# Kernel optimization log

Hardware: AMD Instinct MI355X
Metric: run time of the kernel (lower is better)

Reference implementation:

```python
import jax, jax.numpy as jnp
import numpy as np

B, C, H, W = 32, 512, 32, 32
K = 1024  # num_embeddings


def setup_inputs() -> dict:
    key = jax.random.key(0)
    k1, k2 = jax.random.split(key)
    z = jax.random.normal(k1, (B, C, H, W), dtype=jnp.float32)
    embedding = jax.random.normal(k2, (K, C), dtype=jnp.float32)
    return {"z": z, "embedding": embedding}


def reference(z, embedding):
    # NCHW -> NHWC, flatten to [N, C]
    zt = jnp.transpose(z, (0, 2, 3, 1))            # [B, H, W, C]
    z_flat = zt.reshape(-1, zt.shape[-1])          # [N, C]
    # squared-euclidean distances: ||z||^2 - 2 z.e^T + ||e||^2
    dist = (jnp.sum(z_flat ** 2, axis=1, keepdims=True)
            - 2.0 * z_flat @ embedding.T
            + jnp.sum(embedding ** 2, axis=1))     # [N, K]
    indices = jnp.argmin(dist, axis=1)             # [N]
    quantized = embedding[indices].reshape(zt.shape)  # [B, H, W, C]
    quantized = jnp.transpose(quantized, (0, 3, 1, 2))  # [B, C, H, W]
    return quantized, indices.reshape(z.shape[0], -1)
```

## Files before the change

### kernel.cpp

```cpp
#include <hip/hip_runtime.h>
#include <hip/hip_bf16.h>

#define CDIM 512
#define KDIM 1024
#define HW   1024
#define NPOS 32768
#define BM   128
#define BN   128
#define BK   64
#define NKS  (CDIM / BK)
#define NNB  (KDIM / BN)
#define TILE_USHORT (8 * 128 * 8)

typedef float  f32x16 __attribute__((ext_vector_type(16)));
typedef float  f4     __attribute__((ext_vector_type(4)));
typedef short  bf16x8 __attribute__((ext_vector_type(8)));
typedef unsigned int u32x4 __attribute__((ext_vector_type(4)));

static __device__ __forceinline__ unsigned short f2bf(float f) {
    __hip_bfloat16 h = __float2bfloat16(f);
    union { __hip_bfloat16 h; unsigned short u; } cv; cv.h = h; return cv.u;
}
static __device__ __forceinline__ float bf2f(unsigned short u) {
    union { unsigned short u; __hip_bfloat16 h; } cv; cv.u = u; return __bfloat162float(cv.h);
}

__global__ __launch_bounds__(64) void prep_e(const float* __restrict__ e,
                                             unsigned short* __restrict__ Bt_hi,
                                             unsigned short* __restrict__ Bt_lo,
                                             float* __restrict__ enorm) {
    const int k  = blockIdx.x;
    const int t  = threadIdx.x;
    const int nb = k >> 7, row = k & 127;
    const int ks = t >> 3, slot = t & 7;

    const f4* src = (const f4*)(e + (size_t)k * CDIM + ks * 64 + slot * 8);
    const f4 a = src[0], b = src[1];
    float v[8] = {a.x, a.y, a.z, a.w, b.x, b.y, b.z, b.w};

    unsigned int hw_[4], lw_[4];
    float ss = 0.0f;
    #pragma unroll
    for (int d = 0; d < 4; ++d) {
        const float v0 = v[2 * d], v1 = v[2 * d + 1];
        const unsigned short h0 = f2bf(v0), h1 = f2bf(v1);
        hw_[d] = (unsigned int)h0 | ((unsigned int)h1 << 16);
        lw_[d] = (unsigned int)f2bf(v0 - bf2f(h0)) |
                 ((unsigned int)f2bf(v1 - bf2f(h1)) << 16);
        ss += v0 * v0 + v1 * v1;
    }
    const size_t off = ((((size_t)nb * 8 + ks) * 8 + slot) * 128 + row) * 8;
    *(u32x4*)(Bt_hi + off) = u32x4{hw_[0], hw_[1], hw_[2], hw_[3]};
    *(u32x4*)(Bt_lo + off) = u32x4{lw_[0], lw_[1], lw_[2], lw_[3]};

    #pragma unroll
    for (int o = 32; o > 0; o >>= 1) ss += __shfl_down(ss, o, 64);
    if (t == 0) enorm[k] = ss;
}

__global__ __launch_bounds__(256) void vq_gemm(const float* __restrict__ z,
                                               const unsigned short* __restrict__ Bt_hi,
                                               const unsigned short* __restrict__ Bt_lo,
                                               const float* __restrict__ enorm,
                                               float2* __restrict__ part) {
    __shared__ unsigned short Ah[8][128][8], Al[8][128][8];
    __shared__ unsigned short Bh[8][128][8], Bl[8][128][8];
    __shared__ float lval[2][128];
    __shared__ int   lidx[2][128];

    const int bid = blockIdx.x;
    const int x = bid & 7, jj = bid >> 3;
    const int m  = x * 32 + (jj >> 3);
    const int nb = jj & 7;

    const int n0  = m * BM;
    const int b   = n0 >> 10;
    const int hw0 = n0 & 1023;

    const int t   = threadIdx.x;
    const int wid = t >> 6, l = t & 63;
    const int wr  = wid >> 1, wc = wid & 1;

    f32x16 acc[2][2];
    #pragma unroll
    for (int i = 0; i < 2; ++i)
        #pragma unroll
        for (int j = 0; j < 2; ++j) acc[i][j] = (f32x16)0.0f;

    const float* zbase = z + (size_t)b * CDIM * HW + hw0;
    const int sp = t & 127;
    const int sh = t >> 7;

    for (int ks = 0; ks < NKS; ++ks) {
        float v[32];
        const float* zc = zbase + (size_t)(ks * 64 + sh * 32) * HW + sp;
        #pragma unroll
        for (int i = 0; i < 32; ++i) v[i] = zc[(size_t)i * HW];
        u32x4 bhv[4], blv[4];
        const u32x4* bsh = (const u32x4*)(Bt_hi + ((size_t)nb * 8 + ks) * TILE_USHORT);
        const u32x4* bsl = (const u32x4*)(Bt_lo + ((size_t)nb * 8 + ks) * TILE_USHORT);
        #pragma unroll
        for (int q = 0; q < 4; ++q) { bhv[q] = bsh[q * 256 + t]; blv[q] = bsl[q * 256 + t]; }

        __syncthreads();

        #pragma unroll
        for (int o = 0; o < 4; ++o) {
            unsigned int hw_[4], lw_[4];
            #pragma unroll
            for (int d = 0; d < 4; ++d) {
                const float a0 = v[o * 8 + 2 * d], a1 = v[o * 8 + 2 * d + 1];
                const unsigned short h0 = f2bf(a0), h1 = f2bf(a1);
                hw_[d] = (unsigned int)h0 | ((unsigned int)h1 << 16);
                lw_[d] = (unsigned int)f2bf(a0 - bf2f(h0)) |
                         ((unsigned int)f2bf(a1 - bf2f(h1)) << 16);
            }
            *(u32x4*)&Ah[sh * 4 + o][sp][0] = u32x4{hw_[0], hw_[1], hw_[2], hw_[3]};
            *(u32x4*)&Al[sh * 4 + o][sp][0] = u32x4{lw_[0], lw_[1], lw_[2], lw_[3]};
        }
        unsigned short* bhp = &Bh[0][0][0];
        unsigned short* blp = &Bl[0][0][0];
        #pragma unroll
        for (int q = 0; q < 4; ++q) {
            *(u32x4*)(bhp + (size_t)(q * 256 + t) * 8) = bhv[q];
            *(u32x4*)(blp + (size_t)(q * 256 + t) * 8) = blv[q];
        }
        __syncthreads();

        #pragma unroll
        for (int ksub = 0; ksub < 4; ++ksub) {
            const int so = 2 * ksub + (l >> 5);
            const int cr = wr * 64 + (l & 31);
            const int pr = wc * 64 + (l & 31);
            const bf16x8 ch0 = *(const bf16x8*)&Bh[so][cr][0];
            const bf16x8 ch1 = *(const bf16x8*)&Bh[so][cr + 32][0];
            const bf16x8 cl0 = *(const bf16x8*)&Bl[so][cr][0];
            const bf16x8 cl1 = *(const bf16x8*)&Bl[so][cr + 32][0];
            const bf16x8 ph0 = *(const bf16x8*)&Ah[so][pr][0];
            const bf16x8 ph1 = *(const bf16x8*)&Ah[so][pr + 32][0];
            const bf16x8 pl0 = *(const bf16x8*)&Al[so][pr][0];
            const bf16x8 pl1 = *(const bf16x8*)&Al[so][pr + 32][0];
            acc[0][0] = __builtin_amdgcn_mfma_f32_32x32x16_bf16(ch0, ph0, acc[0][0], 0, 0, 0);
            acc[0][1] = __builtin_amdgcn_mfma_f32_32x32x16_bf16(ch0, ph1, acc[0][1], 0, 0, 0);
            acc[1][0] = __builtin_amdgcn_mfma_f32_32x32x16_bf16(ch1, ph0, acc[1][0], 0, 0, 0);
            acc[1][1] = __builtin_amdgcn_mfma_f32_32x32x16_bf16(ch1, ph1, acc[1][1], 0, 0, 0);
            acc[0][0] = __builtin_amdgcn_mfma_f32_32x32x16_bf16(ch0, pl0, acc[0][0], 0, 0, 0);
            acc[0][1] = __builtin_amdgcn_mfma_f32_32x32x16_bf16(ch0, pl1, acc[0][1], 0, 0, 0);
            acc[1][0] = __builtin_amdgcn_mfma_f32_32x32x16_bf16(ch1, pl0, acc[1][0], 0, 0, 0);
            acc[1][1] = __builtin_amdgcn_mfma_f32_32x32x16_bf16(ch1, pl1, acc[1][1], 0, 0, 0);
            acc[0][0] = __builtin_amdgcn_mfma_f32_32x32x16_bf16(cl0, ph0, acc[0][0], 0, 0, 0);
            acc[0][1] = __builtin_amdgcn_mfma_f32_32x32x16_bf16(cl0, ph1, acc[0][1], 0, 0, 0);
            acc[1][0] = __builtin_amdgcn_mfma_f32_32x32x16_bf16(cl1, ph0, acc[1][0], 0, 0, 0);
            acc[1][1] = __builtin_amdgcn_mfma_f32_32x32x16_bf16(cl1, ph1, acc[1][1], 0, 0, 0);
        }
    }

    const float* en = enorm + nb * 128 + wr * 64;
    #pragma unroll
    for (int pj = 0; pj < 2; ++pj) {
        float bv = 1e30f; int bi = 1 << 20;
        #pragma unroll
        for (int ci = 0; ci < 2; ++ci) {
            #pragma unroll
            for (int r = 0; r < 16; ++r) {
                const int code = ci * 32 + (r & 3) + 8 * (r >> 2) + 4 * (l >> 5);
                const float val = en[code] - 2.0f * acc[ci][pj][r];
                if (val < bv || (val == bv && code < bi)) { bv = val; bi = code; }
            }
        }
        const float ov = __shfl_xor(bv, 32, 64);
        const int   oi = __shfl_xor(bi, 32, 64);
        if (ov < bv || (ov == bv && oi < bi)) { bv = ov; bi = oi; }
        if (l < 32) { lval[wr][wc * 64 + pj * 32 + l] = bv; lidx[wr][wc * 64 + pj * 32 + l] = bi; }
    }
    __syncthreads();

    if (t < 128) {
        const float v0 = lval[0][t]; const int i0 = lidx[0][t];
        const float v1 = lval[1][t]; const int i1 = lidx[1][t] + 64;
        float bv = v0; int bi = i0;
        if (v1 < bv || (v1 == bv && i1 < bi)) { bv = v1; bi = i1; }
        part[(size_t)(n0 + t) * 8 + nb] = make_float2(bv, (float)(nb * 128 + bi));
    }
}

__global__ __launch_bounds__(256) void vq_reduce(const float2* __restrict__ part,
                                                 const float* __restrict__ e,
                                                 float* __restrict__ out_q,
                                                 float* __restrict__ out_i) {
    __shared__ int bidx[128];
    const int t  = threadIdx.x;
    const int p0 = blockIdx.x * 128;

    if (t < 128) {
        const int n = p0 + t;
        const float2* pr = part + (size_t)n * 8;
        float bv = pr[0].x; int bi = (int)pr[0].y;
        #pragma unroll
        for (int nb = 1; nb < 8; ++nb) {
            const float2 c = pr[nb];
            const int ci = (int)c.y;
            if (c.x < bv || (c.x == bv && ci < bi)) { bv = c.x; bi = ci; }
        }
        bidx[t] = bi;
        out_i[n] = (float)bi;
    }
    __syncthreads();

    const int p = t & 127, h = t >> 7;
    const int n = p0 + p;
    const int b = n >> 10, hwp = n & 1023;
    const f4* e4 = (const f4*)(e + (size_t)bidx[p] * CDIM);
    float* oq = out_q + (size_t)b * CDIM * HW + hwp;
    #pragma unroll 4
    for (int j = 0; j < 64; ++j) {
        const f4 vv = e4[h * 64 + j];
        const int c = h * 256 + j * 4;
        oq[(size_t)(c + 0) * HW] = vv.x;
        oq[(size_t)(c + 1) * HW] = vv.y;
        oq[(size_t)(c + 2) * HW] = vv.z;
        oq[(size_t)(c + 3) * HW] = vv.w;
    }
}

extern "C" void kernel_launch(void* const* d_in, const int* in_sizes, int n_in,
                              void* d_out, int out_size, void* d_ws, size_t ws_size,
                              hipStream_t stream) {
    const float* z = (const float*)d_in[0];
    const float* e = (const float*)d_in[1];

    float* out_q = (float*)d_out;
    float* out_i = out_q + (out_size - NPOS);

    unsigned short* Bt_hi = (unsigned short*)d_ws;
    unsigned short* Bt_lo = Bt_hi + (size_t)KDIM * CDIM;
    float*  enorm = (float*)(Bt_lo + (size_t)KDIM * CDIM);
    float2* part  = (float2*)((char*)d_ws + 2 * 1048576 + 4096);

    prep_e<<<KDIM, 64, 0, stream>>>(e, Bt_hi, Bt_lo, enorm);
    vq_gemm<<<(NPOS / BM) * NNB, 256, 0, stream>>>(z, Bt_hi, Bt_lo, enorm, part);
    vq_reduce<<<NPOS / 128, 256, 0, stream>>>(part, e, out_q, out_i);
}
```

Baseline: 231.2 us.

## Prefetch next K-slice into registers and vectorize gather output stores

The GEMM main loop now loads the next z slice and codebook tile into registers right after the shared-memory stores, so global loads overlap the MFMA work on the current slice (register double buffering). The loop is also fully unrolled. Separately, the gather kernel now has each thread handle four consecutive positions and write float4 stores along the spatial dimension instead of scalar strided stores. Both changes raise register pressure, which may lower occupancy.

```diff
diff --git a/kernel.cpp b/kernel.cpp
--- a/kernel.cpp
+++ b/kernel.cpp
@@ -91,17 +91,21 @@
     const int sp = t & 127;
     const int sh = t >> 7;
 
+    float v[32];
+    u32x4 bhv[4], blv[4];
+
+    {
+        const float* zc = zbase + (size_t)(sh * 32) * HW + sp;
+        #pragma unroll
+        for (int i = 0; i < 32; ++i) v[i] = zc[(size_t)i * HW];
+        const u32x4* bsh = (const u32x4*)(Bt_hi + (size_t)nb * 8 * TILE_USHORT);
+        const u32x4* bsl = (const u32x4*)(Bt_lo + (size_t)nb * 8 * TILE_USHORT);
+        #pragma unroll
+        for (int q = 0; q < 4; ++q) { bhv[q] = bsh[q * 256 + t]; blv[q] = bsl[q * 256 + t]; }
+    }
+
+    #pragma unroll
     for (int ks = 0; ks < NKS; ++ks) {
-        float v[32];
-        const float* zc = zbase + (size_t)(ks * 64 + sh * 32) * HW + sp;
-        #pragma unroll
-        for (int i = 0; i < 32; ++i) v[i] = zc[(size_t)i * HW];
-        u32x4 bhv[4], blv[4];
-        const u32x4* bsh = (const u32x4*)(Bt_hi + ((size_t)nb * 8 + ks) * TILE_USHORT);
-        const u32x4* bsl = (const u32x4*)(Bt_lo + ((size_t)nb * 8 + ks) * TILE_USHORT);
-        #pragma unroll
-        for (int q = 0; q < 4; ++q) { bhv[q] = bsh[q * 256 + t]; blv[q] = bsl[q * 256 + t]; }
-
         __syncthreads();
 
         #pragma unroll
@@ -126,6 +130,16 @@
             *(u32x4*)(blp + (size_t)(q * 256 + t) * 8) = blv[q];
         }
         __syncthreads();
+
+        if (ks + 1 < NKS) {
+            const float* zc = zbase + (size_t)((ks + 1) * 64 + sh * 32) * HW + sp;
+            #pragma unroll
+            for (int i = 0; i < 32; ++i) v[i] = zc[(size_t)i * HW];
+            const u32x4* bsh = (const u32x4*)(Bt_hi + ((size_t)nb * 8 + ks + 1) * TILE_USHORT);
+            const u32x4* bsl = (const u32x4*)(Bt_lo + ((size_t)nb * 8 + ks + 1) * TILE_USHORT);
+            #pragma unroll
+            for (int q = 0; q < 4; ++q) { bhv[q] = bsh[q * 256 + t]; blv[q] = bsl[q * 256 + t]; }
+        }
 
         #pragma unroll
         for (int ksub = 0; ksub < 4; ++ksub) {
@@ -207,19 +221,27 @@
     }
     __syncthreads();
 
-    const int p = t & 127, h = t >> 7;
-    const int n = p0 + p;
-    const int b = n >> 10, hwp = n & 1023;
-    const f4* e4 = (const f4*)(e + (size_t)bidx[p] * CDIM);
+    const int pq = t & 31;
+    const int cs = t >> 5;
+    const int n  = p0 + pq * 4;
+    const int b  = n >> 10, hwp = n & 1023;
+
+    const int r0 = bidx[pq * 4 + 0], r1 = bidx[pq * 4 + 1];
+    const int r2 = bidx[pq * 4 + 2], r3 = bidx[pq * 4 + 3];
+    const f4* e0 = (const f4*)(e + (size_t)r0 * CDIM) + cs * 16;
+    const f4* e1 = (const f4*)(e + (size_t)r1 * CDIM) + cs * 16;
+    const f4* e2 = (const f4*)(e + (size_t)r2 * CDIM) + cs * 16;
+    const f4* e3 = (const f4*)(e + (size_t)r3 * CDIM) + cs * 16;
     float* oq = out_q + (size_t)b * CDIM * HW + hwp;
+
     #pragma unroll 4
-    for (int j = 0; j < 64; ++j) {
-        const f4 vv = e4[h * 64 + j];
-        const int c = h * 256 + j * 4;
-        oq[(size_t)(c + 0) * HW] = vv.x;
-        oq[(size_t)(c + 1) * HW] = vv.y;
-        oq[(size_t)(c + 2) * HW] = vv.z;
-        oq[(size_t)(c + 3) * HW] = vv.w;
+    for (int q = 0; q < 16; ++q) {
+        const f4 a = e0[q], bb = e1[q], c = e2[q], d = e3[q];
+        const int cbase = cs * 64 + q * 4;
+        *(f4*)(oq + (size_t)(cbase + 0) * HW) = f4{a.x, bb.x, c.x, d.x};
+        *(f4*)(oq + (size_t)(cbase + 1) * HW) = f4{a.y, bb.y, c.y, d.y};
+        *(f4*)(oq + (size_t)(cbase + 2) * HW) = f4{a.z, bb.z, c.z, d.z};
+        *(f4*)(oq + (size_t)(cbase + 3) * HW) = f4{a.w, bb.w, c.w, d.w};
     }
 }
 
```

Result: slower. 239.3 us (+3.5%).
